# Kernel tuning notes

Hardware: AMD Instinct MI355X
Metric: run time of the kernel (lower is better)

## Reference

```python
import jax, jax.numpy as jnp
import numpy as np

B, S, T, CIN = 8, 256, 4, 4
PATCH, EMBED, DEPTH = 8, 512, 12
NUM_BLOCKS, MODES = 8, 16
OUT_C, OUT_T, OUT_LAYER = 4, 1, 32
N_CLS = 12
E1 = OUT_C * PATCH + 3          # patch-embed intermediate width (35)
BS = EMBED // NUM_BLOCKS        # AFNO block size (64)
GRID = S // PATCH               # 32x32 token grid


def gelu(x):
    return jax.nn.gelu(x, approximate=False)


def group_norm(x, scale, bias, groups=8, eps=1e-5):
    b, h, w, c = x.shape
    xg = x.reshape(b, h, w, groups, c // groups)
    mu = xg.mean(axis=(1, 2, 4), keepdims=True)
    var = xg.var(axis=(1, 2, 4), keepdims=True)
    xg = (xg - mu) * jax.lax.rsqrt(var + eps)
    return xg.reshape(b, h, w, c) * scale + bias


def afno2d(x, w1, b1, w2, b2):
    # x: (b,h,w,c); block-diagonal complex 2-layer MLP on truncated rFFT modes
    b, h, w, c = x.shape
    xf = jnp.fft.rfft2(x, axes=(1, 2), norm='ortho')
    H, Wf = xf.shape[1], xf.shape[2]
    kh, kw = min(MODES, H), min(MODES, Wf)
    xk = xf[:, :kh, :kw].reshape(b, kh, kw, NUM_BLOCKS, BS)
    xr, xi = jnp.real(xk), jnp.imag(xk)
    o1r = gelu(jnp.einsum('...bi,bio->...bo', xr, w1[0]) - jnp.einsum('...bi,bio->...bo', xi, w1[1]) + b1[0])
    o1i = gelu(jnp.einsum('...bi,bio->...bo', xi, w1[0]) + jnp.einsum('...bi,bio->...bo', xr, w1[1]) + b1[1])
    o2r = jnp.einsum('...bi,bio->...bo', o1r, w2[0]) - jnp.einsum('...bi,bio->...bo', o1i, w2[1]) + b2[0]
    o2i = jnp.einsum('...bi,bio->...bo', o1i, w2[0]) + jnp.einsum('...bi,bio->...bo', o1r, w2[1]) + b2[1]
    pad = ((0, 0), (0, H - kh), (0, Wf - kw), (0, 0), (0, 0))
    of = (jnp.pad(o2r, pad) + 1j * jnp.pad(o2i, pad)).reshape(b, H, Wf, c)
    return jnp.fft.irfft2(of, s=(h, w), axes=(1, 2), norm='ortho') + x


def dpot_forward(x, patch_w, patch_b, p1_w, p1_b, pos_embed, tagg_w, tagg_gamma,
                 gn1_s, gn1_b, aw1, ab1, aw2, ab2, gn2_s, gn2_b, mw1, mb1, mw2, mb2,
                 cls_w1, cls_b1, cls_w2, cls_b2, cls_w3, cls_b3,
                 dec_w, dec_b, c3_w, c3_b, c1_w, c1_b):
    b, sx, sy, t, ci = x.shape
    gx = jnp.broadcast_to(jnp.linspace(0., 1., sx, dtype=jnp.float32).reshape(1, sx, 1, 1, 1), (b, sx, sy, t, 1))
    gy = jnp.broadcast_to(jnp.linspace(0., 1., sy, dtype=jnp.float32).reshape(1, 1, sy, 1, 1), (b, sx, sy, t, 1))
    gz = jnp.broadcast_to(jnp.linspace(0., 1., t, dtype=jnp.float32).reshape(1, 1, 1, t, 1), (b, sx, sy, t, 1))
    h = jnp.concatenate([x, gx, gy, gz], axis=-1)
    h = jnp.transpose(h, (0, 3, 1, 2, 4)).reshape(b * t, sx, sy, ci + 3)
    dn = ('NHWC', 'HWIO', 'NHWC')
    # patch embed: strided conv -> gelu -> 1x1 conv
    h = jax.lax.conv_general_dilated(h, patch_w, (PATCH, PATCH), 'VALID', dimension_numbers=dn) + patch_b
    h = gelu(h)
    h = jnp.einsum('bhwc,co->bhwo', h, p1_w[0, 0]) + p1_b
    h = h + pos_embed
    h = h.reshape(b, t, GRID, GRID, EMBED).transpose(0, 2, 3, 1, 4)  # (b,ph,pw,t,e)
    # exp_mlp time aggregation
    temb = jnp.cos(jnp.linspace(0., 1., t, dtype=jnp.float32)[:, None] @ tagg_gamma)  # (t,e)
    h = jnp.einsum('tij,bhwti->bhwj', tagg_w, h * temb)
    for i in range(DEPTH):
        res = h
        z = group_norm(h, gn1_s[i], gn1_b[i])
        z = afno2d(z, aw1[i], ab1[i], aw2[i], ab2[i])
        z = group_norm(z, gn2_s[i], gn2_b[i])
        z = gelu(z @ mw1[i] + mb1[i]) @ mw2[i] + mb2[i]
        h = z + res
    cls_tok = h.mean(axis=(1, 2))
    cp = gelu(cls_tok @ cls_w1 + cls_b1)
    cp = gelu(cp @ cls_w2 + cls_b2)
    cp = cp @ cls_w3 + cls_b3
    y = jax.lax.conv_transpose(h, dec_w, (PATCH, PATCH), 'VALID', dimension_numbers=dn, transpose_kernel=True) + dec_b
    y = gelu(y)
    y = jax.lax.conv_general_dilated(y, c3_w, (1, 1), 'SAME', dimension_numbers=dn) + c3_b
    y = gelu(y)
    y = jnp.einsum('bhwc,co->bhwo', y, c1_w[0, 0]) + c1_b
    y = y.reshape(b, sx, sy, OUT_T, OUT_C)
    return y, cp


def setup_inputs() -> dict:
    key = jax.random.key(0)
    ks = iter(jax.random.split(key, 64))
    u = lambda shape, s=0.02: s * jax.random.normal(next(ks), shape, jnp.float32)
    afno_scale = 1.0 / (BS * BS)
    au = lambda shape: afno_scale * jax.random.uniform(next(ks), shape, dtype=jnp.float32)
    return dict(
        x=jax.random.normal(next(ks), (B, S, S, T, CIN), jnp.float32),
        patch_w=u((PATCH, PATCH, CIN + 3, E1)), patch_b=jnp.zeros((E1,), jnp.float32),
        p1_w=u((1, 1, E1, EMBED)), p1_b=jnp.zeros((EMBED,), jnp.float32),
        pos_embed=u((1, GRID, GRID, EMBED)),
        tagg_w=jax.random.normal(next(ks), (T, EMBED, EMBED), jnp.float32) / (T * EMBED ** 0.5),
        tagg_gamma=(2.0 ** jnp.linspace(-10.0, 10.0, EMBED, dtype=jnp.float32))[None, :],
        gn1_s=jnp.ones((DEPTH, EMBED), jnp.float32), gn1_b=jnp.zeros((DEPTH, EMBED), jnp.float32),
        aw1=au((DEPTH, 2, NUM_BLOCKS, BS, BS)), ab1=au((DEPTH, 2, NUM_BLOCKS, BS)),
        aw2=au((DEPTH, 2, NUM_BLOCKS, BS, BS)), ab2=au((DEPTH, 2, NUM_BLOCKS, BS)),
        gn2_s=jnp.ones((DEPTH, EMBED), jnp.float32), gn2_b=jnp.zeros((DEPTH, EMBED), jnp.float32),
        mw1=u((DEPTH, EMBED, EMBED)), mb1=jnp.zeros((DEPTH, EMBED), jnp.float32),
        mw2=u((DEPTH, EMBED, EMBED)), mb2=jnp.zeros((DEPTH, EMBED), jnp.float32),
        cls_w1=u((EMBED, EMBED)), cls_b1=jnp.zeros((EMBED,), jnp.float32),
        cls_w2=u((EMBED, EMBED)), cls_b2=jnp.zeros((EMBED,), jnp.float32),
        cls_w3=u((EMBED, N_CLS)), cls_b3=jnp.zeros((N_CLS,), jnp.float32),
        dec_w=u((PATCH, PATCH, OUT_LAYER, EMBED)), dec_b=jnp.zeros((OUT_LAYER,), jnp.float32),
        c3_w=u((3, 3, OUT_LAYER, OUT_LAYER)), c3_b=jnp.zeros((OUT_LAYER,), jnp.float32),
        c1_w=u((1, 1, OUT_LAYER, OUT_C * OUT_T)), c1_b=jnp.zeros((OUT_C * OUT_T,), jnp.float32),
    )


def reference(x, patch_w, patch_b, p1_w, p1_b, pos_embed, tagg_w, tagg_gamma,
              gn1_s, gn1_b, aw1, ab1, aw2, ab2, gn2_s, gn2_b, mw1, mb1, mw2, mb2,
              cls_w1, cls_b1, cls_w2, cls_b2, cls_w3, cls_b3,
              dec_w, dec_b, c3_w, c3_b, c1_w, c1_b):
    return dpot_forward(x, patch_w, patch_b, p1_w, p1_b, pos_embed, tagg_w, tagg_gamma,
                        gn1_s, gn1_b, aw1, ab1, aw2, ab2, gn2_s, gn2_b, mw1, mb1, mw2, mb2,
                        cls_w1, cls_b1, cls_w2, cls_b2, cls_w3, cls_b3,
                        dec_w, dec_b, c3_w, c3_b, c1_w, c1_b)
```

## Files before the change

### kernel.cpp

```cpp
#include <hip/hip_runtime.h>
#include <cstddef>

typedef __attribute__((ext_vector_type(8))) short bh8;
typedef __attribute__((ext_vector_type(4))) float f4;

__device__ __forceinline__ float gelu_f(float x){
  return 0.5f * x * (1.0f + erff(x * 0.7071067811865476f));
}

__device__ __forceinline__ unsigned short f2bf(float f){
  unsigned int u = __float_as_uint(f);
  unsigned int r = (u + 0x7FFFu + ((u >> 16) & 1u)) >> 16;
  return (unsigned short)r;
}

__device__ __forceinline__ float bf2f(unsigned short u){
  return __uint_as_float(((unsigned int)u) << 16);
}

__device__ __forceinline__ f4 mfma16(bh8 a, bh8 b, f4 c){
  return __builtin_amdgcn_mfma_f32_16x16x32_bf16(a, b, c, 0, 0, 0);
}

__device__ __forceinline__ void gll16(const unsigned short* src, unsigned short* dst){
  __builtin_amdgcn_global_load_lds(
      (const __attribute__((address_space(1))) unsigned int*)src,
      (__attribute__((address_space(3))) unsigned int*)dst, 16, 0, 0);
}

__device__ __forceinline__ void gn_coef8(const float* pa, const float* sc,
                                         const float* bi, int b, int c,
                                         float& sca, float& sh)
{
  const int g = c >> 6;
  float s1 = 0.f, s2 = 0.f;
  #pragma unroll
  for (int q = 0; q < 8; ++q) {
    s1 += pa[(b * 8 + g) * 8 + q];
    s2 += pa[512 + (b * 8 + g) * 8 + q];
  }
  const float mu = s1 * (1.0f / 65536.0f);
  const float var = s2 * (1.0f / 65536.0f) - mu * mu;
  const float rs = rsqrtf(var + 1e-5f);
  sca = sc[c] * rs;
  sh = bi[c] - mu * sca;
}

#define BG_STAGE(dbuf, kofs, BASE, DST) \
  gll16(BASE + (size_t)sr_ * K + (kofs) + ((ss_ ^ (sr_ & 7)) << 3), &DST[dbuf][tid * 8]);

#define BG_LOADA(kofs) { \
  if (AMODE == 3) { \
    const unsigned short* ap16 = Ab16 + (size_t)sr_ * K + (kofs) + ss_ * 8; \
    const uint4 uv = *(const uint4*)ap16; \
    ra0.x = bf2f((unsigned short)(uv.x & 0xffffu)); ra0.y = bf2f((unsigned short)(uv.x >> 16)); \
    ra0.z = bf2f((unsigned short)(uv.y & 0xffffu)); ra0.w = bf2f((unsigned short)(uv.y >> 16)); \
    ra1.x = bf2f((unsigned short)(uv.z & 0xffffu)); ra1.y = bf2f((unsigned short)(uv.z >> 16)); \
    ra1.z = bf2f((unsigned short)(uv.w & 0xffffu)); ra1.w = bf2f((unsigned short)(uv.w >> 16)); \
  } else { \
    const float* ap_ = Afbase + (size_t)sr_ * K + (kofs) + ss_ * 8; \
    ra0 = *(const float4*)ap_; \
    ra1 = *(const float4*)(ap_ + 4); \
  } \
  if (AMODE >= 2) { \
    const int bb_ = (m0 + sr_) >> 10; \
    const int ch_ = (kofs) + ss_ * 8; \
    const float4 c0_ = *(const float4*)(gnc + bb_ * 512 + ch_); \
    const float4 c1_ = *(const float4*)(gnc + bb_ * 512 + ch_ + 4); \
    const float4 h0_ = *(const float4*)(gnc + 4096 + bb_ * 512 + ch_); \
    const float4 h1_ = *(const float4*)(gnc + 4096 + bb_ * 512 + ch_ + 4); \
    ra0.x = fmaf(ra0.x, c0_.x, h0_.x); ra0.y = fmaf(ra0.y, c0_.y, h0_.y); \
    ra0.z = fmaf(ra0.z, c0_.z, h0_.z); ra0.w = fmaf(ra0.w, c0_.w, h0_.w); \
    ra1.x = fmaf(ra1.x, c1_.x, h1_.x); ra1.y = fmaf(ra1.y, c1_.y, h1_.y); \
    ra1.z = fmaf(ra1.z, c1_.z, h1_.z); ra1.w = fmaf(ra1.w, c1_.w, h1_.w); \
  } }

#define BG_WRITEA(dbuf) { \
  const int slot_ = ss_ ^ (sr_ & 7); \
  bh8 av_; \
  av_[0] = (short)f2bf(ra0.x); av_[1] = (short)f2bf(ra0.y); \
  av_[2] = (short)f2bf(ra0.z); av_[3] = (short)f2bf(ra0.w); \
  av_[4] = (short)f2bf(ra1.x); av_[5] = (short)f2bf(ra1.y); \
  av_[6] = (short)f2bf(ra1.z); av_[7] = (short)f2bf(ra1.w); \
  *(bh8*)(&As[dbuf][sr_ * 64 + slot_ * 8]) = av_; }

template<int AMODE, int OMODE>
__global__ __launch_bounds__(1024)
void k_bgemm(const void* __restrict__ Av, const unsigned short* __restrict__ Bt,
             float* __restrict__ C, unsigned short* __restrict__ OB,
             const float* __restrict__ bias, const float* __restrict__ Res,
             const float* __restrict__ gnc, float* __restrict__ gpart,
             int K, int ldc, int nn)
{
  __shared__ __align__(16) unsigned short As[2][8192];
  __shared__ __align__(16) unsigned short Bs[2][8192];
  const int bid = blockIdx.x, nwg = gridDim.x;
  const int wg = (bid & 7) * (nwg >> 3) + (bid >> 3);
  const int mb = wg / nn;
  const int m0 = mb * 128, n0 = (wg - mb * nn) * 128;
  const int tid = threadIdx.x;
  const int w = tid >> 6, lane = tid & 63;
  const int lr = lane & 15, lh = lane >> 4;
  const int wr = w >> 2, wc = w & 3;
  const int sr_ = tid >> 3, ss_ = tid & 7;
  const unsigned short* Abase = (const unsigned short*)Av + (size_t)m0 * K;
  const unsigned short* Ab16 = (const unsigned short*)Av + (size_t)m0 * K;
  const float* Afbase = (const float*)Av + (size_t)m0 * K;
  const unsigned short* Bbase = Bt + (size_t)n0 * K;
  float4 ra0, ra1;
  f4 acc[2][2] = {};

  const int nt = K >> 6;
  if (AMODE == 0) { BG_STAGE(0, 0, Abase, As) }
  else            { BG_LOADA(0) BG_WRITEA(0) }
  BG_STAGE(0, 0, Bbase, Bs)
  __syncthreads();

  for (int t = 0; t < nt; ++t) {
    const int d = t & 1;
    const bool more = (t + 1 < nt);
    if (more) {
      const int kn = (t + 1) << 6;
      if (AMODE == 0) { BG_STAGE(d ^ 1, kn, Abase, As) }
      else            { BG_LOADA(kn) }
      BG_STAGE(d ^ 1, kn, Bbase, Bs)
    }
    #pragma unroll
    for (int kk = 0; kk < 2; ++kk) {
      bh8 af[2], bf[2];
      #pragma unroll
      for (int mi = 0; mi < 2; ++mi) {
        const int R = wr * 32 + mi * 16 + lr;
        af[mi] = *(const bh8*)((const char*)As[d] + R * 128 + (((kk * 4 + lh) ^ (R & 7)) * 16));
      }
      #pragma unroll
      for (int ni = 0; ni < 2; ++ni) {
        const int R = wc * 32 + ni * 16 + lr;
        bf[ni] = *(const bh8*)((const char*)Bs[d] + R * 128 + (((kk * 4 + lh) ^ (R & 7)) * 16));
      }
      #pragma unroll
      for (int mi = 0; mi < 2; ++mi)
        #pragma unroll
        for (int ni = 0; ni < 2; ++ni)
          acc[mi][ni] = mfma16(af[mi], bf[ni], acc[mi][ni]);
    }
    if (more && AMODE != 0) { BG_WRITEA(d ^ 1) }
    __syncthreads();
  }

  float cs1[2], cs2[2];
  #pragma unroll
  for (int ni = 0; ni < 2; ++ni) {
    const int col_l = wc * 32 + ni * 16 + lr;
    const int col = n0 + col_l;
    float bv = 0.f;
    if (OMODE == 1 || OMODE == 2 || OMODE == 4) bv = bias[col];
    if (OMODE == 3) bv = bias[col & 31];
    float s1 = 0.f, s2 = 0.f;
    #pragma unroll
    for (int mi = 0; mi < 2; ++mi) {
      #pragma unroll
      for (int r = 0; r < 4; ++r) {
        const int row = m0 + wr * 32 + mi * 16 + lh * 4 + r;
        float v = acc[mi][ni][r] + bv;
        if (OMODE == 0) {
          C[(size_t)row * ldc + col] = v;
          s1 += v; s2 += v * v;
        } else if (OMODE == 1) {
          OB[(size_t)row * ldc + col] = f2bf(gelu_f(v));
        } else if (OMODE == 2 || OMODE == 4) {
          const size_t ci = (size_t)row * ldc + col;
          v += Res[ci];
          C[ci] = v;
          s1 += v; s2 += v * v;
        } else {
          v = gelu_f(v);
          const int bb = row >> 10, hw = row & 1023, ii = hw >> 5, jj = hw & 31;
          const int dxy = col >> 5, dy = dxy >> 3, dx = dxy & 7, cc = col & 31;
          OB[(((size_t)(bb * 256 + ii * 8 + dy)) * 256 + jj * 8 + dx) * 32 + cc] = f2bf(v);
        }
      }
    }
    cs1[ni] = s1; cs2[ni] = s2;
  }
  if (OMODE == 0 || OMODE == 2 || OMODE == 4) {
    float* sp = (float*)As;
    const int sub = wr * 4 + lh;
    #pragma unroll
    for (int ni = 0; ni < 2; ++ni) {
      const int col_l = wc * 32 + ni * 16 + lr;
      sp[col_l * 16 + sub] = cs1[ni];
      sp[2048 + col_l * 16 + sub] = cs2[ni];
    }
    __syncthreads();
    if (tid < 128) {
      float s1 = 0.f, s2 = 0.f;
      #pragma unroll
      for (int u = 0; u < 16; ++u) { s1 += sp[tid * 16 + u]; s2 += sp[2048 + tid * 16 + u]; }
      const int b = m0 >> 10, slice = (m0 >> 7) & 7;
      if (OMODE == 4) {
        gpart[(b * 8 + slice) * 512 + n0 + tid] = s1;
      } else {
        #pragma unroll
        for (int sft = 32; sft > 0; sft >>= 1) {
          s1 += __shfl_xor(s1, sft, 64);
          s2 += __shfl_xor(s2, sft, 64);
        }
        if ((tid & 63) == 0) {
          const int g = (n0 >> 6) + (tid >> 6);
          gpart[(b * 8 + g) * 8 + slice] = s1;
          gpart[512 + (b * 8 + g) * 8 + slice] = s2;
        }
      }
    }
  }
}

__global__ __launch_bounds__(512)
void k_modes(unsigned int* __restrict__ AB, const unsigned short* __restrict__ Sb_d,
             const float* __restrict__ SB_d)
{
  __shared__ __align__(16) unsigned int ABs[8192];
  __shared__ __align__(16) unsigned short Ws[2][16384];
  __shared__ __align__(16) unsigned short Ps[8192];
  __shared__ __align__(16) unsigned short O1s[8192];
  __shared__ float ct[512], st[512];
  unsigned short* M2 = (unsigned short*)ABs;

  const int bx = blockIdx.x;
  const int chalf = bx & 1, kh = (bx >> 1) & 15, b = bx >> 5;
  const int tid = threadIdx.x;
  const int w = tid >> 6, lane = tid & 63, lr = lane & 15, lh = lane >> 4;
  unsigned int* ABbase = AB + (((size_t)b * 16 + kh) * 32) * 512 + chalf * 256;

  #pragma unroll
  for (int p = 0; p < 4; ++p) {
    const int q = p * 512 + tid;
    const int x = q >> 6, c4 = (q & 63) * 4;
    gll16((const unsigned short*)(ABbase + (size_t)x * 512 + c4),
          (unsigned short*)&ABs[q * 4]);
  }
  {
    const unsigned short* Wsrc = Sb_d + (size_t)(chalf * 4) * 16384;
    #pragma unroll
    for (int p = 0; p < 4; ++p) {
      const int q = p * 512 + tid;
      const int r = q >> 4, c = q & 15;
      gll16(Wsrc + r * 128 + ((c ^ (r & 7)) << 3), &Ws[0][q * 8]);
    }
  }
  {
    const int k = tid >> 5, xx = tid & 31;
    const float ang = (float)((k * xx) & 31) * 0.19634954084936207f;
    ct[tid] = cosf(ang); st[tid] = sinf(ang);
  }
  __syncthreads();

  const int cc = tid & 255, kwh = tid >> 8;
  {
    float gr[8], gi[8];
    #pragma unroll
    for (int j = 0; j < 8; ++j) { gr[j] = 0.f; gi[j] = 0.f; }
    for (int x = 0; x < 32; ++x) {
      const unsigned int pv = ABs[x * 256 + cc];
      const float vr = bf2f((unsigned short)(pv & 0xffffu));
      const float vi = bf2f((unsigned short)(pv >> 16));
      #pragma unroll
      for (int j = 0; j < 8; ++j) {
        const int kg = kwh * 8 + j;
        const float c_ = ct[kg * 32 + x], s_ = st[kg * 32 + x];
        gr[j] += vr * c_ + vi * s_;
        gi[j] += vi * c_ - vr * s_;
      }
    }
    const int cblk = cc >> 6, ci = cc & 63;
    #pragma unroll
    for (int j = 0; j < 8; ++j) {
      const int kw = kwh * 8 + j;
      const int base = cblk * 2048 + kw * 128;
      const int chr = (ci >> 3) ^ (kw & 7);
      const int chi = ((64 + ci) >> 3) ^ (kw & 7);
      Ps[base + (chr << 3) + (ci & 7)] = f2bf(gr[j] * (1.0f / 32.0f));
      Ps[base + (chi << 3) + (ci & 7)] = f2bf(gi[j] * (1.0f / 32.0f));
    }
  }
  __syncthreads();

  for (int i = 0; i < 8; ++i) {
    if (i + 1 < 8) {
      const int j2 = i + 1;
      const unsigned short* Wsrc = Sb_d + (j2 >= 4 ? 131072 : 0)
                                 + (size_t)(chalf * 4 + (j2 & 3)) * 16384;
      #pragma unroll
      for (int p = 0; p < 4; ++p) {
        const int q = p * 512 + tid;
        const int r = q >> 4, c = q & 15;
        gll16(Wsrc + r * 128 + ((c ^ (r & 7)) << 3), &Ws[j2 & 1][q * 8]);
      }
    }
    const int cblk = i & 3;
    const unsigned short* src = (i < 4) ? Ps : O1s;
    f4 acc = {};
    #pragma unroll
    for (int ks = 0; ks < 4; ++ks) {
      const bh8 a = *(const bh8*)(&src[cblk * 2048 + lr * 128
                      + (((ks * 4 + lh) ^ (lr & 7)) << 3)]);
      const int rw = w * 16 + lr;
      const bh8 bb = *(const bh8*)(&Ws[i & 1][rw * 128
                      + (((ks * 4 + lh) ^ (rw & 7)) << 3)]);
      acc = mfma16(a, bb, acc);
    }
    const int o = w * 16 + lr;
    if (i < 4) {
      const float bv = SB_d[(chalf * 4 + cblk) * 128 + o];
      #pragma unroll
      for (int r = 0; r < 4; ++r) {
        const int kw = lh * 4 + r;
        const int ch = (o >> 3) ^ (kw & 7);
        O1s[cblk * 2048 + kw * 128 + (ch << 3) + (o & 7)] = f2bf(gelu_f(acc[r] + bv));
      }
    } else {
      const float bv = SB_d[1024 + (chalf * 4 + cblk) * 128 + o];
      #pragma unroll
      for (int r = 0; r < 4; ++r) {
        const int kw = lh * 4 + r;
        M2[cblk * 2048 + kw * 128 + o] = f2bf(acc[r] + bv);
      }
    }
    __syncthreads();
  }

  {
    const int xh = tid >> 8;
    const int cblk = cc >> 6, ci = cc & 63;
    float gr[16], gi[16];
    #pragma unroll
    for (int kw = 0; kw < 16; ++kw) {
      const float wf = (kw == 0) ? 1.0f : 2.0f;
      gr[kw] = wf * bf2f(M2[cblk * 2048 + kw * 128 + ci]);
      gi[kw] = wf * bf2f(M2[cblk * 2048 + kw * 128 + 64 + ci]);
    }
    for (int x = xh * 16; x < xh * 16 + 16; ++x) {
      float tr = 0.f, ti = 0.f;
      #pragma unroll
      for (int kw = 0; kw < 16; ++kw) {
        const float c_ = ct[kw * 32 + x], s_ = st[kw * 32 + x];
        tr += gr[kw] * c_ - gi[kw] * s_;
        ti += gi[kw] * c_ + gr[kw] * s_;
      }
      ABbase[(size_t)x * 512 + cc] = (unsigned int)f2bf(tr) | ((unsigned int)f2bf(ti) << 16);
    }
  }
}

__global__ __launch_bounds__(256)
void k_pack(const float* __restrict__ x, unsigned short* __restrict__ imat)
{
  const int nb = blockIdx.x;
  const int j = nb & 31, i = (nb >> 5) & 31, b = nb >> 10;
  const int tid = threadIdx.x;
  const int tl = tid >> 6, px = tid & 63;
  const int dy = px >> 3, dx = px & 7;
  const int Y = i * 8 + dy, X = j * 8 + dx;
  const float4 v = *(const float4*)(x + (((size_t)(b * 256 + Y)) * 256 + X) * 16 + tl * 4);
  const size_t row = (size_t)nb * 4 + tl;
  ushort4 ov;
  ov.x = f2bf(v.x); ov.y = f2bf(v.y); ov.z = f2bf(v.z); ov.w = f2bf(v.w);
  *(ushort4*)(imat + row * 448 + px * 4) = ov;
  for (int q = tid; q < 768; q += 256) {
    const int tt = q / 192, r = q - tt * 192;
    const int sec = r >> 6, p2 = r & 63;
    float val;
    if (sec == 0)      val = (float)(i * 8 + (p2 >> 3)) * (1.0f / 255.0f);
    else if (sec == 1) val = (float)(j * 8 + (p2 & 7)) * (1.0f / 255.0f);
    else               val = (float)tt * (1.0f / 3.0f);
    imat[((size_t)nb * 4 + tt) * 448 + 256 + sec * 64 + p2] = f2bf(val);
  }
}

__global__ __launch_bounds__(256)
void k_prep_btp(const float* __restrict__ pw, const float* __restrict__ pb,
                unsigned short* __restrict__ btp, float* __restrict__ pbp)
{
  const int idx = blockIdx.x * 256 + threadIdx.x;
  if (idx < 28672) {
    const int n = idx / 448, k = idx - (idx / 448) * 448;
    int l;
    if (k < 256) { const int pxx = k >> 2, c = k & 3; l = pxx * 7 + c; }
    else { const int sec = (k - 256) >> 6, p2 = (k - 256) & 63; l = p2 * 7 + 4 + sec; }
    btp[n * 448 + k] = (n < 35) ? f2bf(pw[l * 35 + n]) : (unsigned short)0;
  }
  if (idx < 64) pbp[idx] = (idx < 35) ? pb[idx] : 0.0f;
}

__global__ __launch_bounds__(256)
void k_prep_bte(const float* __restrict__ w, unsigned short* __restrict__ bte)
{
  const int idx = blockIdx.x * 256 + threadIdx.x;
  const int n = idx >> 6, k = idx & 63;
  bte[idx] = (k < 35) ? f2bf(w[k * 512 + n]) : (unsigned short)0;
}

__global__ __launch_bounds__(256)
void k_temb(const float* __restrict__ gamma, float* __restrict__ temb)
{
  const int idx = blockIdx.x * 256 + threadIdx.x;
  const int t = idx >> 9, e = idx & 511;
  temb[idx] = cosf((float)t * (1.0f / 3.0f) * gamma[e]);
}

__global__ __launch_bounds__(256)
void k_cvt_trans(const float* __restrict__ in, unsigned short* __restrict__ out,
                 int K, int N, long long sIn, long long sOut)
{
  __shared__ float tile[32][33];
  const int z = blockIdx.z;
  in  += (size_t)z * sIn;
  out += (size_t)z * sOut;
  const int n0 = blockIdx.x * 32, k0 = blockIdx.y * 32;
  const int tx = threadIdx.x & 31, ty = threadIdx.x >> 5;
  #pragma unroll
  for (int i = 0; i < 4; ++i)
    tile[ty + i * 8][tx] = in[(size_t)(k0 + ty + i * 8) * N + n0 + tx];
  __syncthreads();
  #pragma unroll
  for (int i = 0; i < 4; ++i)
    out[(size_t)(n0 + ty + i * 8) * K + k0 + tx] = f2bf(tile[tx][ty + i * 8]);
}

__global__ __launch_bounds__(256)
void k_cvt(const float* __restrict__ in, unsigned short* __restrict__ out, int n)
{
  const int idx = blockIdx.x * 256 + threadIdx.x;
  if (idx < n) out[idx] = f2bf(in[idx]);
}

__global__ __launch_bounds__(256)
void k_prep_w3(const float* __restrict__ w, unsigned short* __restrict__ out)
{
  const int idx = blockIdx.x * 256 + threadIdx.x;
  if (idx < 9216) {
    const int kb = idx >> 10, co = (idx >> 5) & 31, ci = idx & 31;
    out[idx] = f2bf(w[(kb * 32 + ci) * 32 + co]);
  }
}

template<int BIAS, int GELU, int OMODE>
__global__ __launch_bounds__(256)
void k_mgemm(const unsigned short* __restrict__ A, const unsigned short* __restrict__ Bt,
             const float* __restrict__ bias, unsigned short* __restrict__ OB,
             const float* __restrict__ pos, const float* __restrict__ temb,
             int K, int lda, int ldc,
             long long zsA, long long zsB, long long zsC, int zsBias)
{
  __shared__ __align__(16) unsigned short As[64 * 40];
  __shared__ __align__(16) unsigned short Bs[64 * 40];
  const int z = blockIdx.z;
  A  += (size_t)z * zsA;
  Bt += (size_t)z * zsB;
  if (BIAS) bias += (size_t)z * zsBias;
  OB += (size_t)z * zsC;
  const int m0 = blockIdx.y * 64, n0 = blockIdx.x * 64;
  const int tid = threadIdx.x;
  const int w = tid >> 6, l = tid & 63;
  const int lr = l & 15, lh = l >> 4;
  const int sr = tid >> 2, skq = (tid & 3) * 8;
  f4 acc[4] = {};
  for (int k0 = 0; k0 < K; k0 += 32) {
    const uint4 av = *(const uint4*)(A + (size_t)(m0 + sr) * lda + k0 + skq);
    *(uint4*)(&As[sr * 40 + skq]) = av;
    const uint4 bv = *(const uint4*)(Bt + (size_t)(n0 + sr) * K + k0 + skq);
    *(uint4*)(&Bs[sr * 40 + skq]) = bv;
    __syncthreads();
    const bh8 af = *(const bh8*)(&As[(w * 16 + lr) * 40 + lh * 8]);
    #pragma unroll
    for (int ct = 0; ct < 4; ++ct) {
      const bh8 bf = *(const bh8*)(&Bs[(ct * 16 + lr) * 40 + lh * 8]);
      acc[ct] = mfma16(af, bf, acc[ct]);
    }
    __syncthreads();
  }
  #pragma unroll
  for (int ct = 0; ct < 4; ++ct) {
    const int col = n0 + ct * 16 + lr;
    float bv = 0.f;
    if (BIAS) bv = bias[col];
    #pragma unroll
    for (int r = 0; r < 4; ++r) {
      const int row = m0 + w * 16 + lh * 4 + r;
      float v = acc[ct][r] + bv;
      if (GELU) v = gelu_f(v);
      if (OMODE == 2) {
        const int hw = (row >> 2) & 1023, t = row & 3;
        v = (v + pos[(size_t)hw * 512 + col]) * temb[t * 512 + col];
        OB[(size_t)row * 512 + col] = f2bf(v);
      } else {
        OB[(size_t)row * ldc + col] = f2bf(v);
      }
    }
  }
}

__global__ __launch_bounds__(256)
void k_tail(const unsigned short* __restrict__ Y1, const unsigned short* __restrict__ w3t,
            const float* __restrict__ c1w, const float* __restrict__ c1b,
            float* __restrict__ outp)
{
  __shared__ __align__(16) char lbuf[256 * 33 * 4];
  __shared__ float c1s[128];
  unsigned short* it = (unsigned short*)lbuf;
  float* y2 = (float*)lbuf;
  const int bx = blockIdx.x;
  const int b = bx >> 8, ty = (bx >> 4) & 15, tx = bx & 15;
  const int Y0 = ty * 16, X0 = tx * 16;
  const int tid = threadIdx.x;
  const int w = tid >> 6, l = tid & 63, lr = l & 15, lh = l >> 4;

  if (tid < 128) c1s[tid] = c1w[tid];
  for (int idx = tid; idx < 1296; idx += 256) {
    const int r = idx / 72, rem = idx - r * 72, c = rem >> 2, q = rem & 3;
    const int Yg = Y0 + r - 1, Xg = X0 + c - 1;
    uint4 v = make_uint4(0u, 0u, 0u, 0u);
    if (Yg >= 0 && Yg < 256 && Xg >= 0 && Xg < 256)
      v = *(const uint4*)(Y1 + (((size_t)(b * 256 + Yg)) * 256 + Xg) * 32 + q * 8);
    *(uint4*)(&it[(r * 18 + c) * 40 + q * 8]) = v;
  }
  bh8 bw[2][9];
  #pragma unroll
  for (int ct = 0; ct < 2; ++ct)
    #pragma unroll
    for (int kb = 0; kb < 9; ++kb)
      bw[ct][kb] = *(const bh8*)(w3t + (size_t)(kb * 32 + ct * 16 + lr) * 32 + lh * 8);
  __syncthreads();

  f4 acc[4][2] = {};
  #pragma unroll
  for (int kb = 0; kb < 9; ++kb) {
    const int dy = kb / 3, dx = kb % 3;
    #pragma unroll
    for (int yy = 0; yy < 4; ++yy) {
      const int y = w * 4 + yy;
      const bh8 af = *(const bh8*)(&it[((y + dy) * 18 + lr + dx) * 40 + lh * 8]);
      acc[yy][0] = mfma16(af, bw[0][kb], acc[yy][0]);
      acc[yy][1] = mfma16(af, bw[1][kb], acc[yy][1]);
    }
  }
  __syncthreads();
  #pragma unroll
  for (int yy = 0; yy < 4; ++yy) {
    const int y = w * 4 + yy;
    #pragma unroll
    for (int ct = 0; ct < 2; ++ct)
      #pragma unroll
      for (int r = 0; r < 4; ++r)
        y2[(y * 16 + lh * 4 + r) * 33 + ct * 16 + lr] = gelu_f(acc[yy][ct][r]);
  }
  __syncthreads();
  const int py = tid >> 4, px = tid & 15;
  float o0 = c1b[0], o1 = c1b[1], o2 = c1b[2], o3 = c1b[3];
  #pragma unroll 8
  for (int ci = 0; ci < 32; ++ci) {
    const float v = y2[tid * 33 + ci];
    o0 = fmaf(v, c1s[ci * 4 + 0], o0);
    o1 = fmaf(v, c1s[ci * 4 + 1], o1);
    o2 = fmaf(v, c1s[ci * 4 + 2], o2);
    o3 = fmaf(v, c1s[ci * 4 + 3], o3);
  }
  float4 ov; ov.x = o0; ov.y = o1; ov.z = o2; ov.w = o3;
  *(float4*)(outp + (((size_t)(b * 256 + Y0 + py)) * 256 + X0 + px) * 4) = ov;
}

__global__ __launch_bounds__(256)
void k_dft_a(const float* __restrict__ H, const float* __restrict__ PA,
             const float* __restrict__ sc, const float* __restrict__ bi,
             unsigned int* __restrict__ AB)
{
  __shared__ float ct[512], st[512];
  const int tid = threadIdx.x;
  for (int q = tid; q < 512; q += 256) {
    const int k = q >> 5, y = q & 31;
    const float ang = (float)((k * y) & 31) * 0.19634954084936207f;
    ct[q] = cosf(ang); st[q] = sinf(ang);
  }
  __syncthreads();
  const int blk = blockIdx.x;
  const int kh8 = blk & 1, half = (blk >> 1) & 1, x = (blk >> 2) & 31, b = blk >> 7;
  const int c = half * 256 + tid;
  float sca, sh;
  gn_coef8(PA, sc, bi, b, c, sca, sh);
  float ar[8], ai[8];
  #pragma unroll
  for (int k = 0; k < 8; ++k) { ar[k] = 0.f; ai[k] = 0.f; }
  const float* zp = H + ((size_t)b * 1024 + x) * 512 + c;
  for (int y = 0; y < 32; ++y) {
    const float v = fmaf(zp[(size_t)y * 32 * 512], sca, sh);
    #pragma unroll
    for (int k = 0; k < 8; ++k) {
      const int kg = kh8 * 8 + k;
      ar[k] = fmaf(v, ct[kg * 32 + y], ar[k]);
      ai[k] = fmaf(-v, st[kg * 32 + y], ai[k]);
    }
  }
  #pragma unroll
  for (int k = 0; k < 8; ++k) {
    const int kg = kh8 * 8 + k;
    const size_t o = (((size_t)b * 16 + kg) * 32 + x) * 512 + c;
    AB[o] = (unsigned int)f2bf(ar[k]) | ((unsigned int)f2bf(ai[k]) << 16);
  }
}

__global__ __launch_bounds__(256)
void k_mode_prep_all(const float* __restrict__ aw1, const float* __restrict__ aw2,
                     const float* __restrict__ ab1, const float* __restrict__ ab2,
                     unsigned short* __restrict__ Sb, float* __restrict__ SB)
{
  const int gi = blockIdx.x * 256 + threadIdx.x;
  const int dd = gi >> 18;
  const int idx = gi & 262143;
  const float* aw1_d = aw1 + (size_t)dd * 65536;
  const float* aw2_d = aw2 + (size_t)dd * 65536;
  const int s = idx >> 17;
  const int blk = (idx >> 14) & 7;
  const int n = (idx >> 7) & 127;
  const int kk = idx & 127;
  const float* aw = s ? aw2_d : aw1_d;
  const int i = kk & 63, o = n & 63;
  const float wr = aw[(blk * 64 + i) * 64 + o];
  const float wi = aw[32768 + (blk * 64 + i) * 64 + o];
  float val;
  if (n < 64) val = (kk < 64) ? wr : -wi;
  else        val = (kk < 64) ? wi :  wr;
  Sb[gi] = f2bf(val);
  if (idx < 2048) {
    const int s2 = idx >> 10, r2 = idx & 1023, b2 = r2 >> 7, q2 = r2 & 127;
    const float* ab = s2 ? (ab2 + dd * 1024) : (ab1 + dd * 1024);
    SB[dd * 2048 + idx] = (q2 < 64) ? ab[b2 * 64 + q2] : ab[512 + b2 * 64 + (q2 - 64)];
  }
}

__global__ __launch_bounds__(256)
void k_idft_e(const unsigned int* __restrict__ Tp, const float* __restrict__ H,
              const float* __restrict__ PA, const float* __restrict__ sc,
              const float* __restrict__ bi, unsigned short* __restrict__ zab,
              float* __restrict__ PB)
{
  __shared__ float ct[512], st[512];
  const int tid = threadIdx.x;
  for (int q = tid; q < 512; q += 256) {
    const int k = q >> 5, y = q & 31;
    const float ang = (float)((k * y) & 31) * 0.19634954084936207f;
    ct[q] = cosf(ang); st[q] = sinf(ang);
  }
  __syncthreads();
  const int blk = blockIdx.x;
  const int yh = blk & 1, half = (blk >> 1) & 1, x = (blk >> 2) & 31, b = blk >> 7;
  const int c = half * 256 + tid;
  float sca, sh;
  gn_coef8(PA, sc, bi, b, c, sca, sh);
  float trv[16], tiv[16];
  #pragma unroll
  for (int k = 0; k < 16; ++k) {
    const size_t o = (((size_t)b * 16 + k) * 32 + x) * 512 + c;
    const unsigned int pv = Tp[o];
    trv[k] = bf2f((unsigned short)(pv & 0xffffu));
    tiv[k] = bf2f((unsigned short)(pv >> 16));
  }
  float s1 = 0.f, s2 = 0.f;
  for (int y = yh * 16; y < yh * 16 + 16; ++y) {
    float v = 0.f;
    #pragma unroll
    for (int k = 0; k < 16; ++k)
      v += trv[k] * ct[k * 32 + y] - tiv[k] * st[k * 32 + y];
    const size_t o = ((size_t)b * 1024 + y * 32 + x) * 512 + c;
    const float zv = v * (1.0f / 32.0f) + fmaf(H[o], sca, sh);
    zab[o] = f2bf(zv);
    s1 += zv; s2 += zv * zv;
  }
  #pragma unroll
  for (int sft = 32; sft > 0; sft >>= 1) {
    s1 += __shfl_xor(s1, sft, 64);
    s2 += __shfl_xor(s2, sft, 64);
  }
  if ((tid & 63) == 0) {
    const int g = half * 4 + (tid >> 6);
    PB[(b * 8 + g) * 64 + x * 2 + yh] = s1;
    PB[4096 + (b * 8 + g) * 64 + x * 2 + yh] = s2;
  }
}

__global__ __launch_bounds__(256)
void k_gn_coef(const float* __restrict__ PB, const float* __restrict__ sc,
               const float* __restrict__ bi, float* __restrict__ gnc)
{
  const int idx = blockIdx.x * 256 + threadIdx.x;
  const int b = idx >> 9, c = idx & 511, g = c >> 6;
  float s1 = 0.f, s2 = 0.f;
  #pragma unroll
  for (int q = 0; q < 64; ++q) {
    s1 += PB[(b * 8 + g) * 64 + q];
    s2 += PB[4096 + (b * 8 + g) * 64 + q];
  }
  const float mu = s1 * (1.0f / 65536.0f);
  const float var = s2 * (1.0f / 65536.0f) - mu * mu;
  const float rs = rsqrtf(var + 1e-5f);
  const float sca = sc[c] * rs;
  gnc[idx] = sca;
  gnc[4096 + idx] = bi[c] - mu * sca;
}

template<int FIRST>
__global__ __launch_bounds__(256)
void k_cls_l(const float* __restrict__ src, const float* __restrict__ Wm,
             const float* __restrict__ bb, float* __restrict__ Cout)
{
  __shared__ float tok[512];
  __shared__ float red[256];
  const int b = blockIdx.y, oc = blockIdx.x;
  const int tid = threadIdx.x;
  for (int i = tid; i < 512; i += 256) {
    if (FIRST) {
      float s = 0.f;
      #pragma unroll
      for (int q = 0; q < 8; ++q) s += src[((b * 8 + q) << 9) + i];
      tok[i] = s * (1.0f / 1024.0f);
    } else {
      tok[i] = src[b * 512 + i];
    }
  }
  __syncthreads();
  const int to = tid & 63, iq = tid >> 6;
  const int o = oc * 64 + to;
  const float* wp = Wm + (size_t)(iq * 128) * 512 + o;
  const float* tp = tok + iq * 128;
  float a0 = 0.f, a1 = 0.f, a2 = 0.f, a3 = 0.f;
  #pragma unroll 8
  for (int i = 0; i < 128; i += 4) {
    a0 = fmaf(tp[i + 0], wp[(size_t)(i + 0) * 512], a0);
    a1 = fmaf(tp[i + 1], wp[(size_t)(i + 1) * 512], a1);
    a2 = fmaf(tp[i + 2], wp[(size_t)(i + 2) * 512], a2);
    a3 = fmaf(tp[i + 3], wp[(size_t)(i + 3) * 512], a3);
  }
  red[tid] = (a0 + a1) + (a2 + a3);
  __syncthreads();
  if (tid < 64) {
    const int oo = oc * 64 + tid;
    const float v = red[tid] + red[tid + 64] + red[tid + 128] + red[tid + 192] + bb[oo];
    Cout[b * 512 + oo] = gelu_f(v);
  }
}

__global__ __launch_bounds__(768)
void k_cls3(const float* __restrict__ C2, const float* __restrict__ w3,
            const float* __restrict__ b3, float* __restrict__ outp)
{
  const int b = blockIdx.x, tid = threadIdx.x;
  const int o = tid >> 6, lane = tid & 63;
  float acc = 0.f;
  for (int i = lane; i < 512; i += 64)
    acc = fmaf(C2[b * 512 + i], w3[i * 12 + o], acc);
  #pragma unroll
  for (int s = 32; s > 0; s >>= 1) acc += __shfl_xor(acc, s, 64);
  if (lane == 0) outp[2097152 + b * 12 + o] = acc + b3[o];
}

extern "C" void kernel_launch(void* const* d_in, const int* in_sizes, int n_in,
                              void* d_out, int out_size, void* d_ws, size_t ws_size,
                              hipStream_t stream)
{
  (void)in_sizes; (void)n_in; (void)out_size; (void)ws_size;
  const float* x      = (const float*)d_in[0];
  const float* patch_w= (const float*)d_in[1];
  const float* patch_b= (const float*)d_in[2];
  const float* p1_w   = (const float*)d_in[3];
  const float* p1_b   = (const float*)d_in[4];
  const float* pos    = (const float*)d_in[5];
  const float* tagg_w = (const float*)d_in[6];
  const float* gamma  = (const float*)d_in[7];
  const float* gn1_s  = (const float*)d_in[8];
  const float* gn1_b  = (const float*)d_in[9];
  const float* aw1    = (const float*)d_in[10];
  const float* ab1    = (const float*)d_in[11];
  const float* aw2    = (const float*)d_in[12];
  const float* ab2    = (const float*)d_in[13];
  const float* gn2_s  = (const float*)d_in[14];
  const float* gn2_b  = (const float*)d_in[15];
  const float* mw1    = (const float*)d_in[16];
  const float* mb1    = (const float*)d_in[17];
  const float* mw2    = (const float*)d_in[18];
  const float* mb2    = (const float*)d_in[19];
  const float* cls_w1 = (const float*)d_in[20];
  const float* cls_b1 = (const float*)d_in[21];
  const float* cls_w2 = (const float*)d_in[22];
  const float* cls_b2 = (const float*)d_in[23];
  const float* cls_w3 = (const float*)d_in[24];
  const float* cls_b3 = (const float*)d_in[25];
  const float* dec_w  = (const float*)d_in[26];
  const float* dec_b  = (const float*)d_in[27];
  const float* c3_w   = (const float*)d_in[28];
  const float* c3_b   = (const float*)d_in[29];
  const float* c1_w   = (const float*)d_in[30];
  const float* c1_b   = (const float*)d_in[31];

  float* W = (float*)d_ws;
  float* H            = W;
  unsigned int* ABT   = (unsigned int*)(W + 4194304);
  unsigned short* UO  = (unsigned short*)(W + 8388608);
  float* R1           = W + 10485760;
  unsigned short* SbA = (unsigned short*)(W + 18874368);
  float* SBa          = W + 20447232;
  unsigned short* taggT = (unsigned short*)(W + 20471808);
  unsigned short* mwT1  = (unsigned short*)(W + 20996096);
  unsigned short* mwT2  = (unsigned short*)(W + 22568960);
  unsigned short* decC  = (unsigned short*)(W + 24141824);
  unsigned short* w3t   = (unsigned short*)(W + 24666112);
  unsigned short* btp   = (unsigned short*)(W + 24674304);
  unsigned short* bte   = (unsigned short*)(W + 24688640);
  float* TEMB  = W + 24705024;
  float* PBP   = W + 24707072;
  float* PA    = W + 24707136;
  float* PB    = W + 24708160;
  float* GNC   = W + 24716352;
  float* PARTC = W + 24724544;
  float* C1    = W + 24757312;
  float* C2    = W + 24761408;

  unsigned short* imat = (unsigned short*)R1;
  unsigned short* H0b  = (unsigned short*)R1;
  unsigned short* Y1   = (unsigned short*)R1;
  unsigned short* ZAb  = (unsigned short*)R1;
  unsigned short* P1b = UO;
  unsigned short* Ub  = UO;
  float* out = (float*)d_out;

  k_cvt_trans<<<dim3(16,64,1),256,0,stream>>>(tagg_w, taggT, 2048, 512, 0, 0);
  k_cvt_trans<<<dim3(16,16,12),256,0,stream>>>(mw1, mwT1, 512, 512, 262144, 262144);
  k_cvt_trans<<<dim3(16,16,12),256,0,stream>>>(mw2, mwT2, 512, 512, 262144, 262144);
  k_cvt<<<4096,256,0,stream>>>(dec_w, decC, 1048576);
  k_prep_w3<<<36,256,0,stream>>>(c3_w, w3t);
  k_prep_btp<<<112,256,0,stream>>>(patch_w, patch_b, btp, PBP);
  k_prep_bte<<<128,256,0,stream>>>(p1_w, bte);
  k_temb<<<8,256,0,stream>>>(gamma, TEMB);
  k_mode_prep_all<<<12288,256,0,stream>>>(aw1, aw2, ab1, ab2, SbA, SBa);

  k_pack<<<8192,256,0,stream>>>(x, imat);
  k_mgemm<1,1,1><<<dim3(1,512),256,0,stream>>>(imat, btp, PBP, P1b,
      nullptr, nullptr, 448, 448, 64, 0, 0, 0, 0);
  k_mgemm<1,0,2><<<dim3(8,512),256,0,stream>>>(P1b, bte, p1_b, H0b,
      pos, TEMB, 64, 64, 512, 0, 0, 0, 0);
  k_bgemm<0,0><<<256,1024,0,stream>>>(H0b, taggT, H, nullptr, nullptr, nullptr,
      nullptr, PA, 2048, 512, 4);

  for (int d = 0; d < 12; ++d) {
    k_dft_a<<<1024,256,0,stream>>>(H, PA, gn1_s + d*512, gn1_b + d*512, ABT);
    k_modes<<<256,512,0,stream>>>(ABT, SbA + (size_t)d*262144, SBa + d*2048);
    k_idft_e<<<1024,256,0,stream>>>(ABT, H, PA, gn1_s + d*512, gn1_b + d*512, ZAb, PB);
    k_gn_coef<<<16,256,0,stream>>>(PB, gn2_s + d*512, gn2_b + d*512, GNC);
    k_bgemm<3,1><<<256,1024,0,stream>>>(ZAb, mwT1 + (size_t)d*262144, nullptr, Ub,
        mb1 + d*512, nullptr, GNC, nullptr, 512, 512, 4);
    if (d < 11)
      k_bgemm<0,2><<<256,1024,0,stream>>>(Ub, mwT2 + (size_t)d*262144, H, nullptr,
          mb2 + d*512, H, nullptr, PA, 512, 512, 4);
    else
      k_bgemm<0,4><<<256,1024,0,stream>>>(Ub, mwT2 + (size_t)d*262144, H, nullptr,
          mb2 + d*512, H, nullptr, PARTC, 512, 512, 4);
  }

  k_cls_l<1><<<dim3(8,8),256,0,stream>>>(PARTC, cls_w1, cls_b1, C1);
  k_cls_l<0><<<dim3(8,8),256,0,stream>>>(C1, cls_w2, cls_b2, C2);
  k_cls3<<<8,768,0,stream>>>(C2, cls_w3, cls_b3, out);
  k_bgemm<1,3><<<1024,1024,0,stream>>>(H, decC, nullptr, Y1,
      dec_b, nullptr, nullptr, nullptr, 512, 0, 16);
  k_tail<<<2048,256,0,stream>>>(Y1, w3t, c1_w, c1_b, out);
}
```

Before: 1.187 ms.

## Fuse GroupNorm coefficient computation into MLP GEMM and split mode kernel finer

```diff
diff --git a/kernel.cpp b/kernel.cpp
--- a/kernel.cpp
+++ b/kernel.cpp
@@ -50,7 +50,7 @@
   gll16(BASE + (size_t)sr_ * K + (kofs) + ((ss_ ^ (sr_ & 7)) << 3), &DST[dbuf][tid * 8]);
 
 #define BG_LOADA(kofs) { \
-  if (AMODE == 3) { \
+  if (AMODE == 3 || AMODE == 4) { \
     const unsigned short* ap16 = Ab16 + (size_t)sr_ * K + (kofs) + ss_ * 8; \
     const uint4 uv = *(const uint4*)ap16; \
     ra0.x = bf2f((unsigned short)(uv.x & 0xffffu)); ra0.y = bf2f((unsigned short)(uv.x >> 16)); \
@@ -62,7 +62,7 @@
     ra0 = *(const float4*)ap_; \
     ra1 = *(const float4*)(ap_ + 4); \
   } \
-  if (AMODE >= 2) { \
+  if (AMODE == 2 || AMODE == 3) { \
     const int bb_ = (m0 + sr_) >> 10; \
     const int ch_ = (kofs) + ss_ * 8; \
     const float4 c0_ = *(const float4*)(gnc + bb_ * 512 + ch_); \
@@ -73,6 +73,17 @@
     ra0.z = fmaf(ra0.z, c0_.z, h0_.z); ra0.w = fmaf(ra0.w, c0_.w, h0_.w); \
     ra1.x = fmaf(ra1.x, c1_.x, h1_.x); ra1.y = fmaf(ra1.y, c1_.y, h1_.y); \
     ra1.z = fmaf(ra1.z, c1_.z, h1_.z); ra1.w = fmaf(ra1.w, c1_.w, h1_.w); \
+  } \
+  if (AMODE == 4) { \
+    const int ch_ = (kofs) + ss_ * 8; \
+    const float4 c0_ = *(const float4*)(gncs + ch_); \
+    const float4 c1_ = *(const float4*)(gncs + ch_ + 4); \
+    const float4 h0_ = *(const float4*)(gncs + 512 + ch_); \
+    const float4 h1_ = *(const float4*)(gncs + 512 + ch_ + 4); \
+    ra0.x = fmaf(ra0.x, c0_.x, h0_.x); ra0.y = fmaf(ra0.y, c0_.y, h0_.y); \
+    ra0.z = fmaf(ra0.z, c0_.z, h0_.z); ra0.w = fmaf(ra0.w, c0_.w, h0_.w); \
+    ra1.x = fmaf(ra1.x, c1_.x, h1_.x); ra1.y = fmaf(ra1.y, c1_.y, h1_.y); \
+    ra1.z = fmaf(ra1.z, c1_.z, h1_.z); ra1.w = fmaf(ra1.w, c1_.w, h1_.w); \
   } }
 
 #define BG_WRITEA(dbuf) { \
@@ -94,6 +105,7 @@
 {
   __shared__ __align__(16) unsigned short As[2][8192];
   __shared__ __align__(16) unsigned short Bs[2][8192];
+  __shared__ __align__(16) float gncs[1024];
   const int bid = blockIdx.x, nwg = gridDim.x;
   const int wg = (bid & 7) * (nwg >> 3) + (bid >> 3);
   const int mb = wg / nn;
@@ -109,6 +121,25 @@
   const unsigned short* Bbase = Bt + (size_t)n0 * K;
   float4 ra0, ra1;
   f4 acc[2][2] = {};
+
+  if (AMODE == 4) {
+    if (tid < 512) {
+      const int bq = m0 >> 10, g = tid >> 6;
+      float s1 = 0.f, s2 = 0.f;
+      #pragma unroll
+      for (int q = 0; q < 64; ++q) {
+        s1 += gnc[(bq * 8 + g) * 64 + q];
+        s2 += gnc[4096 + (bq * 8 + g) * 64 + q];
+      }
+      const float mu = s1 * (1.0f / 65536.0f);
+      const float var = s2 * (1.0f / 65536.0f) - mu * mu;
+      const float rs = rsqrtf(var + 1e-5f);
+      const float sca = Res[tid] * rs;
+      gncs[tid] = sca;
+      gncs[512 + tid] = gpart[tid] - mu * sca;
+    }
+    __syncthreads();
+  }
 
   const int nt = K >> 6;
   if (AMODE == 0) { BG_STAGE(0, 0, Abase, As) }
@@ -216,53 +247,53 @@
   }
 }
 
-__global__ __launch_bounds__(512)
+__global__ __launch_bounds__(256)
 void k_modes(unsigned int* __restrict__ AB, const unsigned short* __restrict__ Sb_d,
              const float* __restrict__ SB_d)
 {
-  __shared__ __align__(16) unsigned int ABs[8192];
-  __shared__ __align__(16) unsigned short Ws[2][16384];
-  __shared__ __align__(16) unsigned short Ps[8192];
-  __shared__ __align__(16) unsigned short O1s[8192];
+  __shared__ __align__(16) unsigned int ABs[4096];
+  __shared__ __align__(16) unsigned short Ws[16384];
+  __shared__ __align__(16) unsigned short Ps[4096];
+  __shared__ __align__(16) unsigned short O1s[4096];
   __shared__ float ct[512], st[512];
   unsigned short* M2 = (unsigned short*)ABs;
 
   const int bx = blockIdx.x;
-  const int chalf = bx & 1, kh = (bx >> 1) & 15, b = bx >> 5;
+  const int cq = bx & 3, kh = (bx >> 2) & 15, b = bx >> 6;
   const int tid = threadIdx.x;
   const int w = tid >> 6, lane = tid & 63, lr = lane & 15, lh = lane >> 4;
-  unsigned int* ABbase = AB + (((size_t)b * 16 + kh) * 32) * 512 + chalf * 256;
+  unsigned int* ABbase = AB + (((size_t)b * 16 + kh) * 32) * 512 + cq * 128;
 
   #pragma unroll
   for (int p = 0; p < 4; ++p) {
-    const int q = p * 512 + tid;
-    const int x = q >> 6, c4 = (q & 63) * 4;
+    const int q = p * 256 + tid;
+    const int x = q >> 5, c4 = (q & 31) * 4;
     gll16((const unsigned short*)(ABbase + (size_t)x * 512 + c4),
           (unsigned short*)&ABs[q * 4]);
   }
   {
-    const unsigned short* Wsrc = Sb_d + (size_t)(chalf * 4) * 16384;
-    #pragma unroll
-    for (int p = 0; p < 4; ++p) {
-      const int q = p * 512 + tid;
+    const unsigned short* Wsrc = Sb_d + (size_t)(cq * 2) * 16384;
+    #pragma unroll
+    for (int p = 0; p < 8; ++p) {
+      const int q = p * 256 + tid;
       const int r = q >> 4, c = q & 15;
-      gll16(Wsrc + r * 128 + ((c ^ (r & 7)) << 3), &Ws[0][q * 8]);
-    }
-  }
-  {
-    const int k = tid >> 5, xx = tid & 31;
+      gll16(Wsrc + r * 128 + ((c ^ (r & 7)) << 3), &Ws[q * 8]);
+    }
+  }
+  for (int q = tid; q < 512; q += 256) {
+    const int k = q >> 5, xx = q & 31;
     const float ang = (float)((k * xx) & 31) * 0.19634954084936207f;
-    ct[tid] = cosf(ang); st[tid] = sinf(ang);
-  }
-  __syncthreads();
-
-  const int cc = tid & 255, kwh = tid >> 8;
+    ct[q] = cosf(ang); st[q] = sinf(ang);
+  }
+  __syncthreads();
+
+  const int cc = tid & 127, kwh = tid >> 7;
   {
     float gr[8], gi[8];
     #pragma unroll
     for (int j = 0; j < 8; ++j) { gr[j] = 0.f; gi[j] = 0.f; }
     for (int x = 0; x < 32; ++x) {
-      const unsigned int pv = ABs[x * 256 + cc];
+      const unsigned int pv = ABs[x * 128 + cc];
       const float vr = bf2f((unsigned short)(pv & 0xffffu));
       const float vi = bf2f((unsigned short)(pv >> 16));
       #pragma unroll
@@ -286,52 +317,59 @@
   }
   __syncthreads();
 
-  for (int i = 0; i < 8; ++i) {
-    if (i + 1 < 8) {
-      const int j2 = i + 1;
-      const unsigned short* Wsrc = Sb_d + (j2 >= 4 ? 131072 : 0)
-                                 + (size_t)(chalf * 4 + (j2 & 3)) * 16384;
-      #pragma unroll
-      for (int p = 0; p < 4; ++p) {
-        const int q = p * 512 + tid;
-        const int r = q >> 4, c = q & 15;
-        gll16(Wsrc + r * 128 + ((c ^ (r & 7)) << 3), &Ws[j2 & 1][q * 8]);
-      }
-    }
-    const int cblk = i & 3;
-    const unsigned short* src = (i < 4) ? Ps : O1s;
-    f4 acc = {};
+  for (int i = 0; i < 4; ++i) {
+    const int cblk = i & 1;
+    const unsigned short* src = (i < 2) ? Ps : O1s;
+    f4 acc[2] = {};
     #pragma unroll
     for (int ks = 0; ks < 4; ++ks) {
       const bh8 a = *(const bh8*)(&src[cblk * 2048 + lr * 128
                       + (((ks * 4 + lh) ^ (lr & 7)) << 3)]);
-      const int rw = w * 16 + lr;
-      const bh8 bb = *(const bh8*)(&Ws[i & 1][rw * 128
-                      + (((ks * 4 + lh) ^ (rw & 7)) << 3)]);
-      acc = mfma16(a, bb, acc);
-    }
-    const int o = w * 16 + lr;
-    if (i < 4) {
-      const float bv = SB_d[(chalf * 4 + cblk) * 128 + o];
-      #pragma unroll
-      for (int r = 0; r < 4; ++r) {
-        const int kw = lh * 4 + r;
-        const int ch = (o >> 3) ^ (kw & 7);
-        O1s[cblk * 2048 + kw * 128 + (ch << 3) + (o & 7)] = f2bf(gelu_f(acc[r] + bv));
-      }
-    } else {
-      const float bv = SB_d[1024 + (chalf * 4 + cblk) * 128 + o];
-      #pragma unroll
-      for (int r = 0; r < 4; ++r) {
-        const int kw = lh * 4 + r;
-        M2[cblk * 2048 + kw * 128 + o] = f2bf(acc[r] + bv);
+      #pragma unroll
+      for (int j = 0; j < 2; ++j) {
+        const int rw = (w * 2 + j) * 16 + lr;
+        const bh8 bb = *(const bh8*)(&Ws[rw * 128 + (((ks * 4 + lh) ^ (rw & 7)) << 3)]);
+        acc[j] = mfma16(a, bb, acc[j]);
+      }
+    }
+    const int z = cq * 2 + cblk;
+    #pragma unroll
+    for (int j = 0; j < 2; ++j) {
+      const int o = (w * 2 + j) * 16 + lr;
+      if (i < 2) {
+        const float bv = SB_d[z * 128 + o];
+        #pragma unroll
+        for (int r = 0; r < 4; ++r) {
+          const int kw = lh * 4 + r;
+          const int ch = (o >> 3) ^ (kw & 7);
+          O1s[cblk * 2048 + kw * 128 + (ch << 3) + (o & 7)] = f2bf(gelu_f(acc[j][r] + bv));
+        }
+      } else {
+        const float bv = SB_d[1024 + z * 128 + o];
+        #pragma unroll
+        for (int r = 0; r < 4; ++r) {
+          const int kw = lh * 4 + r;
+          M2[cblk * 2048 + kw * 128 + o] = f2bf(acc[j][r] + bv);
+        }
       }
     }
     __syncthreads();
+    if (i < 3) {
+      const int j2 = i + 1;
+      const unsigned short* Wsrc = Sb_d + (j2 >= 2 ? 131072 : 0)
+                                 + (size_t)(cq * 2 + (j2 & 1)) * 16384;
+      #pragma unroll
+      for (int p = 0; p < 8; ++p) {
+        const int q = p * 256 + tid;
+        const int r = q >> 4, c = q & 15;
+        gll16(Wsrc + r * 128 + ((c ^ (r & 7)) << 3), &Ws[q * 8]);
+      }
+      __syncthreads();
+    }
   }
 
   {
-    const int xh = tid >> 8;
+    const int xh = tid >> 7;
     const int cblk = cc >> 6, ci = cc & 63;
     float gr[16], gi[16];
     #pragma unroll
@@ -686,26 +724,6 @@
     PB[(b * 8 + g) * 64 + x * 2 + yh] = s1;
     PB[4096 + (b * 8 + g) * 64 + x * 2 + yh] = s2;
   }
-}
-
-__global__ __launch_bounds__(256)
-void k_gn_coef(const float* __restrict__ PB, const float* __restrict__ sc,
-               const float* __restrict__ bi, float* __restrict__ gnc)
-{
-  const int idx = blockIdx.x * 256 + threadIdx.x;
-  const int b = idx >> 9, c = idx & 511, g = c >> 6;
-  float s1 = 0.f, s2 = 0.f;
-  #pragma unroll
-  for (int q = 0; q < 64; ++q) {
-    s1 += PB[(b * 8 + g) * 64 + q];
-    s2 += PB[4096 + (b * 8 + g) * 64 + q];
-  }
-  const float mu = s1 * (1.0f / 65536.0f);
-  const float var = s2 * (1.0f / 65536.0f) - mu * mu;
-  const float rs = rsqrtf(var + 1e-5f);
-  const float sca = sc[c] * rs;
-  gnc[idx] = sca;
-  gnc[4096 + idx] = bi[c] - mu * sca;
 }
 
 template<int FIRST>
@@ -819,10 +837,9 @@
   float* PBP   = W + 24707072;
   float* PA    = W + 24707136;
   float* PB    = W + 24708160;
-  float* GNC   = W + 24716352;
-  float* PARTC = W + 24724544;
-  float* C1    = W + 24757312;
-  float* C2    = W + 24761408;
+  float* PARTC = W + 24716352;
+  float* C1    = W + 24749120;
+  float* C2    = W + 24753216;
 
   unsigned short* imat = (unsigned short*)R1;
   unsigned short* H0b  = (unsigned short*)R1;
@@ -852,11 +869,10 @@
 
   for (int d = 0; d < 12; ++d) {
     k_dft_a<<<1024,256,0,stream>>>(H, PA, gn1_s + d*512, gn1_b + d*512, ABT);
-    k_modes<<<256,512,0,stream>>>(ABT, SbA + (size_t)d*262144, SBa + d*2048);
+    k_modes<<<512,256,0,stream>>>(ABT, SbA + (size_t)d*262144, SBa + d*2048);
     k_idft_e<<<1024,256,0,stream>>>(ABT, H, PA, gn1_s + d*512, gn1_b + d*512, ZAb, PB);
-    k_gn_coef<<<16,256,0,stream>>>(PB, gn2_s + d*512, gn2_b + d*512, GNC);
-    k_bgemm<3,1><<<256,1024,0,stream>>>(ZAb, mwT1 + (size_t)d*262144, nullptr, Ub,
-        mb1 + d*512, nullptr, GNC, nullptr, 512, 512, 4);
+    k_bgemm<4,1><<<256,1024,0,stream>>>(ZAb, mwT1 + (size_t)d*262144, nullptr, Ub,
+        mb1 + d*512, gn2_s + d*512, PB, const_cast<float*>(gn2_b) + d*512, 512, 512, 4);
     if (d < 11)
       k_bgemm<0,2><<<256,1024,0,stream>>>(Ub, mwT2 + (size_t)d*262144, H, nullptr,
           mb2 + d*512, H, nullptr, PA, 512, 512, 4);
```

After: 1.137 ms. 1.04x faster.
